# Performance work log

Hardware: AMD Instinct MI355X
Metric: run time of the kernel (lower is better)

## Reference

```python
import jax, jax.numpy as jnp
import numpy as np

T, B, E, H, V = 128, 64, 300, 2048, 50000


def setup_inputs() -> dict:
    key = jax.random.key(0)
    ks = jax.random.split(key, 7)
    tokens = jax.random.randint(ks[0], (T, B), 0, V, dtype=jnp.int32)
    lens = jax.random.randint(ks[1], (B,), 1, T + 1, dtype=jnp.int32)  # lens >= 1 (assert 0 not in lens)
    embed_table = jax.random.normal(ks[2], (V, E), dtype=jnp.float32) * 0.1
    W_ih = jax.random.normal(ks[3], (4 * H, E), dtype=jnp.float32) * 0.02
    W_hh = jax.random.normal(ks[4], (4 * H, H), dtype=jnp.float32) * 0.02
    b_ih = jax.random.normal(ks[5], (4 * H,), dtype=jnp.float32) * 0.02
    b_hh = jax.random.normal(ks[6], (4 * H,), dtype=jnp.float32) * 0.02
    return {"tokens": tokens, "lens": lens, "embed_table": embed_table,
            "W_ih": W_ih, "W_hh": W_hh, "b_ih": b_ih, "b_hh": b_hh}


def _lstm_scan(xs, W_ih, W_hh, bias, reverse):
    # xs: [T, B, E]; returns all hidden states [T, B, H] (in scan order) and final (h, c)
    hdim = W_hh.shape[1]
    bsz = xs.shape[1]
    h0 = jnp.zeros((bsz, hdim), xs.dtype)
    c0 = jnp.zeros((bsz, hdim), xs.dtype)

    def step(carry, x):
        h, c = carry
        gates = x @ W_ih.T + h @ W_hh.T + bias  # [B, 4H]
        i, f, g, o = jnp.split(gates, 4, axis=-1)  # PyTorch LSTMCell gate order: i, f, g, o
        i = jax.nn.sigmoid(i)
        f = jax.nn.sigmoid(f)
        g = jnp.tanh(g)
        o = jax.nn.sigmoid(o)
        c = f * c + i * g
        h = o * jnp.tanh(c)
        return (h, c), h

    (h_fin, c_fin), hs = jax.lax.scan(step, (h0, c0), xs, reverse=reverse)
    return hs, h_fin


def reference(tokens, lens, embed_table, W_ih, W_hh, b_ih, b_hh):
    # tokens: [T, B] int ids (time-major, matching input_[i] loop over dim 0)
    x = embed_table[tokens]  # [T, B, E]
    bias = b_ih + b_hh
    hs_fwd, _ = _lstm_scan(x, W_ih, W_hh, bias, reverse=False)   # [T, B, H]
    _, h_bwd = _lstm_scan(x, W_ih, W_hh, bias, reverse=True)     # [B, H], same shared cell
    bsz = tokens.shape[1]
    # forward hidden at the last valid timestep of each example (lens - 1)
    last_fwd = hs_fwd[lens - 1, jnp.arange(bsz)]  # [B, H]
    return jnp.concatenate([last_fwd, h_bwd], axis=1)  # [B, 2H]
```

## Files before the change

### kernel.cpp

```cpp
#include <hip/hip_runtime.h>
#include <math.h>

#define T_ 128
#define B_ 64
#define E_ 300
#define H_ 2048

#define K1   2368
#define XKS  10
#define NKS  74
#define APELEMS 19398656ull
#define BXELEMS 5242880ull
#define BHPING  524288ull

typedef __attribute__((ext_vector_type(8))) short short8;
typedef __attribute__((ext_vector_type(4))) float float4v;

__device__ __forceinline__ unsigned f2bf(float f) {
    unsigned u = __float_as_uint(f);
    return (u + 0x7FFFu + ((u >> 16) & 1u)) >> 16;
}
__device__ __forceinline__ float bf2f(unsigned b) { return __uint_as_float(b << 16); }

__device__ __forceinline__ void gl_lds16(const void* g, void* l) {
    __builtin_amdgcn_global_load_lds(
        (const __attribute__((address_space(1))) unsigned int*)g,
        (__attribute__((address_space(3))) unsigned int*)l, 16, 0, 0);
}

__device__ __forceinline__ float sigm(float x) { return 1.f / (1.f + expf(-x)); }


__global__ void init2(short* __restrict__ Bh, float* __restrict__ cb) {
    const int nB = 2 * (int)BHPING;
    const int nC = 2 * 2048 * 64;
    int stride = gridDim.x * blockDim.x;
    int i = blockIdx.x * blockDim.x + threadIdx.x;
    for (int idx = i; idx < nB; idx += stride) Bh[idx] = 0;
    for (int idx = i; idx < nC; idx += stride) cb[idx] = 0.f;
}

__global__ void pack_w(const float* __restrict__ Wih, const float* __restrict__ Whh,
                       short* __restrict__ Ahi, short* __restrict__ Alo) {
    long long idx = (long long)blockIdx.x * blockDim.x + threadIdx.x;
    if (idx >= (long long)APELEMS) return;
    int j  = (int)(idx & 7);
    int l  = (int)((idx >> 3) & 63);
    int mf = (int)((idx >> 9) & 7);
    int rest = (int)(idx >> 12);
    int ks = rest % 74;
    int rb = rest / 74;
    int row = rb * 128 + mf * 16 + (l & 15);
    int kr  = ks * 32 + (l >> 4) * 8 + j;
    float wv = 0.f;
    if (kr < 300)       wv = Wih[(size_t)row * 300 + kr];
    else if (kr >= 320) wv = Whh[(size_t)row * 2048 + (kr - 320)];
    unsigned hb = f2bf(wv);
    Ahi[idx] = (short)hb;
    Alo[idx] = (short)f2bf(wv - bf2f(hb));
}

__global__ void pack_x(const int* __restrict__ tokens, const float* __restrict__ embed,
                       short* __restrict__ Bx) {
    long long idx = (long long)blockIdx.x * blockDim.x + threadIdx.x;
    if (idx >= (long long)BXELEMS) return;
    int j   = (int)(idx & 7);
    int l   = (int)((idx >> 3) & 63);
    int nf4 = (int)((idx >> 9) & 3);
    int hl  = (int)((idx >> 11) & 1);
    int rest = (int)(idx >> 12);
    int ks = rest % 10;
    int tt = rest / 10;
    int b  = nf4 * 16 + (l & 15);
    int kr = ks * 32 + (l >> 4) * 8 + j;
    float v = 0.f;
    if (kr < 300) {
        int tok = tokens[tt * 64 + b];
        v = embed[(size_t)tok * 300 + kr];
    }
    unsigned hb = f2bf(v);
    Bx[idx] = hl ? (short)f2bf(v - bf2f(hb)) : (short)hb;
}

__global__ __launch_bounds__(256, 2) void gemm_step(
    const short* __restrict__ Ahi, const short* __restrict__ Alo,
    const short* __restrict__ Bx, const short* __restrict__ Bh,
    float* __restrict__ p, int t)
{
    __shared__ short lds[24576];
    const int bb = (int)blockIdx.x;
    const int mb = bb >> 2, s = bb & 3;
    const int rb = mb >> 1, half = mb & 1;
    const int tid = (int)threadIdx.x;
    const int w = tid >> 6, l = tid & 63;
    const int wm = w >> 1, wn = w & 1;
    const int ping = t & 1;
    const int ks0 = (s < 2) ? s * 19 : 38 + (s - 2) * 18;
    const int nks = (s < 2) ? 19 : 18;
    const short* AhiB = Ahi + (size_t)rb * 74 * 4096 + half * 2048;
    const short* AloB = Alo + (size_t)rb * 74 * 4096 + half * 2048;
    const short* BhP  = Bh + (size_t)ping * BHPING;

    float4v acc[2][4];
#pragma unroll
    for (int i = 0; i < 2; ++i)
#pragma unroll
        for (int n = 0; n < 4; ++n) acc[i][n] = (float4v){0.f, 0.f, 0.f, 0.f};

    auto stage = [&](int ks, int buf) {
        short* As = lds + buf * 12288;
        short* Al = As + 2048;
        short* Bs = As + 4096;
        gl_lds16(AhiB + (size_t)ks * 4096 + tid * 8, As + tid * 8);
        gl_lds16(AloB + (size_t)ks * 4096 + tid * 8, Al + tid * 8);
#pragma unroll
        for (int q = 0; q < 4; ++q) {
            const int dsel = q >> 1, hl = q & 1;
            const short* base;
            if (ks < XKS) {
                const int xt = dsel ? (127 - t) : t;
                base = Bx + (size_t)(((xt * 10 + ks) * 2 + hl) * 4) * 512;
            } else {
                base = BhP + (size_t)((ks - 10) * 16 + (dsel * 2 + hl) * 4) * 512;
            }
            gl_lds16(base + tid * 8, Bs + q * 2048 + tid * 8);
        }
    };

    stage(ks0, 0);
    for (int it = 0; it < nks; ++it) {
        asm volatile("s_waitcnt vmcnt(0)" ::: "memory");
        __builtin_amdgcn_s_barrier();
        __builtin_amdgcn_sched_barrier(0);

        short* As = lds + (it & 1) * 12288;
        short* Al = As + 2048;
        short* Bs = As + 4096;
        short8 ah[2], al[2], bf[8];
#pragma unroll
        for (int i = 0; i < 2; ++i) {
            ah[i] = *(const short8*)(As + ((wm * 2 + i) * 64 + l) * 8);
            al[i] = *(const short8*)(Al + ((wm * 2 + i) * 64 + l) * 8);
        }
#pragma unroll
        for (int j = 0; j < 8; ++j)
            bf[j] = *(const short8*)(Bs + ((wn * 8 + j) * 64 + l) * 8);

        stage(ks0 + it + 1, (it + 1) & 1);

        __builtin_amdgcn_s_setprio(1);
#pragma unroll
        for (int i = 0; i < 2; ++i)
#pragma unroll
            for (int h2 = 0; h2 < 2; ++h2)
#pragma unroll
                for (int n = 0; n < 4; ++n)
                    acc[i][n] = __builtin_amdgcn_mfma_f32_16x16x32_bf16(
                        ah[i], bf[h2 * 4 + n], acc[i][n], 0, 0, 0);
#pragma unroll
        for (int i = 0; i < 2; ++i)
#pragma unroll
            for (int n = 0; n < 4; ++n)
                acc[i][n] = __builtin_amdgcn_mfma_f32_16x16x32_bf16(
                    al[i], bf[n], acc[i][n], 0, 0, 0);
        __builtin_amdgcn_s_setprio(0);
    }
    asm volatile("s_waitcnt vmcnt(0)" ::: "memory");
    __builtin_amdgcn_s_barrier();
    __builtin_amdgcn_sched_barrier(0);

#pragma unroll
    for (int i = 0; i < 2; ++i)
#pragma unroll
        for (int n = 0; n < 4; ++n)
#pragma unroll
            for (int r = 0; r < 4; ++r) {
                int row = mb * 64 + wm * 32 + i * 16 + (l >> 4) * 4 + r;
                int col = wn * 64 + n * 16 + (l & 15);
                p[((size_t)s * 8192 + row) * 128 + col] = acc[i][n][r];
            }
}

__global__ __launch_bounds__(256) void update2(
    const float* __restrict__ p,
    const float* __restrict__ b_ih, const float* __restrict__ b_hh,
    const int* __restrict__ lens,
    float* __restrict__ cbuf,
    short* __restrict__ Bh,
    float* __restrict__ out, int t)
{
    int tid0 = blockIdx.x * 256 + threadIdx.x;
    for (int item = tid0; item < 262144; item += 65536) {
        int b = item & 63, k = (item >> 6) & 2047, dir = item >> 17;
        float g[4];
#pragma unroll
        for (int gg = 0; gg < 4; ++gg) {
            int row = gg * 2048 + k;
            float v = 0.f;
#pragma unroll
            for (int s = 0; s < 4; ++s) v += p[((size_t)s * 8192 + row) * 128 + dir * 64 + b];
            g[gg] = v + b_ih[row] + b_hh[row];
        }
        float iv = sigm(g[0]);
        float fv = sigm(g[1]);
        float gv = tanhf(g[2]);
        float ov = sigm(g[3]);
        size_t cidx = ((size_t)dir * 2048 + k) * 64 + b;
        float c = fv * cbuf[cidx] + iv * gv;
        cbuf[cidx] = c;
        float h = ov * tanhf(c);

        int kk = k & 31, ksh = k >> 5;
        int jj = kk & 7, ll = (kk >> 3) * 16 + (b & 15), sub = b >> 4;
        int pingW = (t + 1) & 1;
        size_t baseh = (size_t)pingW * BHPING + ((size_t)ksh * 16 + (dir * 2) * 4 + sub) * 512 + ll * 8 + jj;
        size_t basel = (size_t)pingW * BHPING + ((size_t)ksh * 16 + (dir * 2 + 1) * 4 + sub) * 512 + ll * 8 + jj;
        unsigned hb = f2bf(h);
        Bh[baseh] = (short)hb;
        Bh[basel] = (short)f2bf(h - bf2f(hb));

        if (dir == 0) { if (t == lens[b] - 1) out[(size_t)b * 4096 + k] = h; }
        else          { if (t == 127)         out[(size_t)b * 4096 + 2048 + k] = h; }
    }
}

__global__ void init_state(float* __restrict__ hbuf, float* __restrict__ cbuf) {
    int n_h = 2 * 2 * H_ * B_;
    int n_c = 2 * H_ * B_;
    int stride = gridDim.x * blockDim.x;
    int i = blockIdx.x * blockDim.x + threadIdx.x;
    for (int idx = i; idx < n_h; idx += stride) hbuf[idx] = 0.f;
    for (int idx = i; idx < n_c; idx += stride) cbuf[idx] = 0.f;
}

__global__ void gather_x(const int* __restrict__ tokens, const float* __restrict__ embed,
                         float* __restrict__ x_t) {
    int idx = blockIdx.x * blockDim.x + threadIdx.x;
    int total = T_ * E_ * B_;
    if (idx >= total) return;
    int b = idx % B_;
    int r = idx / B_;
    int e = r % E_;
    int t = r / E_;
    int tok = tokens[t * B_ + b];
    x_t[idx] = embed[tok * E_ + e];
}

__global__ __launch_bounds__(256) void lstm_step(
    const float* __restrict__ x_t, const float* __restrict__ W_ih,
    const float* __restrict__ W_hh, const float* __restrict__ b_ih,
    const float* __restrict__ b_hh, const int* __restrict__ lens,
    const float* __restrict__ h_in, float* __restrict__ h_out,
    float* __restrict__ cbuf, float* __restrict__ out, int t)
{
    const int dir = blockIdx.x >> 8;
    const int kblk = blockIdx.x & 255;
    const int bpair = threadIdx.x & 31;
    const int kloc = threadIdx.x >> 5;
    const int k = kblk * 8 + kloc;
    const int b0 = bpair * 2;
    const int xt = dir ? (T_ - 1 - t) : t;
    const float* xrow = x_t + (size_t)xt * E_ * B_;
    const float* hrow = h_in + (size_t)dir * H_ * B_;
    float a0x = 0.f, a0y = 0.f, a1x = 0.f, a1y = 0.f;
    float a2x = 0.f, a2y = 0.f, a3x = 0.f, a3y = 0.f;
    {
        const float* w0 = W_ih + (size_t)(0 * H_ + k) * E_;
        const float* w1 = W_ih + (size_t)(1 * H_ + k) * E_;
        const float* w2 = W_ih + (size_t)(2 * H_ + k) * E_;
        const float* w3 = W_ih + (size_t)(3 * H_ + k) * E_;
#pragma unroll 4
        for (int kk = 0; kk < E_; ++kk) {
            float2 xv = *(const float2*)(xrow + kk * B_ + b0);
            float c0 = w0[kk], c1 = w1[kk], c2 = w2[kk], c3 = w3[kk];
            a0x += xv.x * c0; a0y += xv.y * c0;
            a1x += xv.x * c1; a1y += xv.y * c1;
            a2x += xv.x * c2; a2y += xv.y * c2;
            a3x += xv.x * c3; a3y += xv.y * c3;
        }
    }
    {
        const float* w0 = W_hh + (size_t)(0 * H_ + k) * H_;
        const float* w1 = W_hh + (size_t)(1 * H_ + k) * H_;
        const float* w2 = W_hh + (size_t)(2 * H_ + k) * H_;
        const float* w3 = W_hh + (size_t)(3 * H_ + k) * H_;
#pragma unroll 4
        for (int kk = 0; kk < H_; ++kk) {
            float2 hv = *(const float2*)(hrow + kk * B_ + b0);
            float c0 = w0[kk], c1 = w1[kk], c2 = w2[kk], c3 = w3[kk];
            a0x += hv.x * c0; a0y += hv.y * c0;
            a1x += hv.x * c1; a1y += hv.y * c1;
            a2x += hv.x * c2; a2y += hv.y * c2;
            a3x += hv.x * c3; a3y += hv.y * c3;
        }
    }
    const int j0 = 0 * H_ + k, j1 = 1 * H_ + k, j2 = 2 * H_ + k, j3 = 3 * H_ + k;
    const float bi = b_ih[j0] + b_hh[j0];
    const float bf = b_ih[j1] + b_hh[j1];
    const float bg = b_ih[j2] + b_hh[j2];
    const float bo = b_ih[j3] + b_hh[j3];
    float* cdir = cbuf + (size_t)dir * H_ * B_;
    float* hdir = h_out + (size_t)dir * H_ * B_;
#pragma unroll
    for (int s = 0; s < 2; ++s) {
        const int b = b0 + s;
        const float ai = (s == 0) ? a0x : a0y;
        const float af = (s == 0) ? a1x : a1y;
        const float ag = (s == 0) ? a2x : a2y;
        const float ao = (s == 0) ? a3x : a3y;
        const float iv = sigm(ai + bi);
        const float fv = sigm(af + bf);
        const float gv = tanhf(ag + bg);
        const float ov = sigm(ao + bo);
        const int sidx = k * B_ + b;
        const float c_old = cdir[sidx];
        const float c_new = fv * c_old + iv * gv;
        cdir[sidx] = c_new;
        const float h_new = ov * tanhf(c_new);
        hdir[sidx] = h_new;
        if (dir == 0) {
            if (t == lens[b] - 1) out[(size_t)b * (2 * H_) + k] = h_new;
        } else {
            if (t == T_ - 1) out[(size_t)b * (2 * H_) + H_ + k] = h_new;
        }
    }
}

extern "C" void kernel_launch(void* const* d_in, const int* in_sizes, int n_in,
                              void* d_out, int out_size, void* d_ws, size_t ws_size,
                              hipStream_t stream) {
    const int*   tokens = (const int*)d_in[0];
    const int*   lens   = (const int*)d_in[1];
    const float* embed  = (const float*)d_in[2];
    const float* W_ih   = (const float*)d_in[3];
    const float* W_hh   = (const float*)d_in[4];
    const float* b_ih   = (const float*)d_in[5];
    const float* b_hh   = (const float*)d_in[6];
    float* out = (float*)d_out;

    short* Ahi = (short*)d_ws;
    short* Alo = Ahi + APELEMS;
    short* BxP = Alo + APELEMS;
    short* BhP = BxP + BXELEMS;
    float* cb2n = (float*)(BhP + 2 * BHPING);
    float* pP   = cb2n + 262144;
    const size_t req_new = (size_t)((char*)(pP + 4194304) - (char*)d_ws);

    float* ws   = (float*)d_ws;
    float* x_t  = ws;
    float* hbuf1 = x_t + (size_t)T_ * E_ * B_;
    float* cbuf1 = hbuf1 + (size_t)2 * 2 * H_ * B_;

    if (ws_size >= req_new) {
        init2<<<512, 256, 0, stream>>>(BhP, cb2n);
        pack_w<<<(int)((APELEMS + 255) / 256), 256, 0, stream>>>(W_ih, W_hh, Ahi, Alo);
        pack_x<<<(int)((BXELEMS + 255) / 256), 256, 0, stream>>>(tokens, embed, BxP);
        for (int t = 0; t < T_; ++t) {
            gemm_step<<<512, 256, 0, stream>>>(Ahi, Alo, BxP, BhP, pP, t);
            update2<<<256, 256, 0, stream>>>(pP, b_ih, b_hh, lens, cb2n, BhP, out, t);
        }
    } else {
        init_state<<<256, 256, 0, stream>>>(hbuf1, cbuf1);
        {
            int total = T_ * E_ * B_;
            gather_x<<<(total + 255) / 256, 256, 0, stream>>>(tokens, embed, x_t);
        }
        for (int t = 0; t < T_; ++t) {
            const float* h_in  = hbuf1 + (size_t)(t & 1) * 2 * H_ * B_;
            float*       h_out = hbuf1 + (size_t)((t + 1) & 1) * 2 * H_ * B_;
            lstm_step<<<512, 256, 0, stream>>>(x_t, W_ih, W_hh, b_ih, b_hh, lens,
                                               h_in, h_out, cbuf1, out, t);
        }
    }
}
```

Baseline: 3.395 ms.

## Compute the weight low-residual correction term with scaled FP8 MFMA

The bf16 low part of the weights (the residual after bf16 rounding) is now stored as scaled e4m3 FP8, and the Alo*Bhi correction product runs through fp8 MFMA into a separate accumulator that is rescaled and added at the end. Separate fp8 copies of the x and h high parts are produced by pack_x and update2 for this purpose. The aim is to halve the bytes loaded for the Alo operand and to use the faster fp8 MFMA, at the cost of extra fp8 conversion work in update2, more LDS, and lower precision in the correction term.

After: 3.537 ms. 4.2% more time.

```diff
diff --git a/kernel.cpp b/kernel.cpp
--- a/kernel.cpp
+++ b/kernel.cpp
@@ -11,7 +11,11 @@
 #define NKS  74
 #define APELEMS 19398656ull
 #define BXELEMS 5242880ull
+#define BXFBYTES 2621440ull
 #define BHPING  524288ull
+#define BHFPING 262144ull
+#define LOSCALE 16384.f
+#define LOINV   6.103515625e-05f
 
 typedef __attribute__((ext_vector_type(8))) short short8;
 typedef __attribute__((ext_vector_type(4))) float float4v;
@@ -21,6 +25,25 @@
     return (u + 0x7FFFu + ((u >> 16) & 1u)) >> 16;
 }
 __device__ __forceinline__ float bf2f(unsigned b) { return __uint_as_float(b << 16); }
+
+__device__ __forceinline__ unsigned char f2e4m3(float f) {
+    unsigned u = __float_as_uint(f);
+    unsigned s = (u >> 31) << 7;
+    u &= 0x7FFFFFFFu;
+    float a = __uint_as_float(u);
+    if (a >= 448.f) return (unsigned char)(s | 0x7E);
+    int e = (int)(u >> 23) - 127;
+    if (e < -6) {
+        int k = (int)(a * 512.f + 0.5f);
+        return (unsigned char)(s | (k <= 7 ? k : 8));
+    }
+    unsigned m = u & 0x7FFFFFu;
+    unsigned mr = m + 0x7FFFFu + ((m >> 20) & 1u);
+    if (mr >> 23) { mr = 0; e += 1; if (e > 8) return (unsigned char)(s | 0x7E); }
+    unsigned mm = (mr >> 20) & 7u;
+    if (e == 8 && mm == 7u) return (unsigned char)(s | 0x7E);
+    return (unsigned char)(s | ((unsigned)(e + 7) << 3) | mm);
+}
 
 __device__ __forceinline__ void gl_lds16(const void* g, void* l) {
     __builtin_amdgcn_global_load_lds(
@@ -31,17 +54,20 @@
 __device__ __forceinline__ float sigm(float x) { return 1.f / (1.f + expf(-x)); }
 
 
-__global__ void init2(short* __restrict__ Bh, float* __restrict__ cb) {
+__global__ void init2(short* __restrict__ Bh, unsigned char* __restrict__ BhF,
+                      float* __restrict__ cb) {
     const int nB = 2 * (int)BHPING;
+    const int nF = 2 * (int)BHFPING;
     const int nC = 2 * 2048 * 64;
     int stride = gridDim.x * blockDim.x;
     int i = blockIdx.x * blockDim.x + threadIdx.x;
     for (int idx = i; idx < nB; idx += stride) Bh[idx] = 0;
+    for (int idx = i; idx < nF; idx += stride) BhF[idx] = 0;
     for (int idx = i; idx < nC; idx += stride) cb[idx] = 0.f;
 }
 
 __global__ void pack_w(const float* __restrict__ Wih, const float* __restrict__ Whh,
-                       short* __restrict__ Ahi, short* __restrict__ Alo) {
+                       short* __restrict__ Ahi, unsigned char* __restrict__ AloF) {
     long long idx = (long long)blockIdx.x * blockDim.x + threadIdx.x;
     if (idx >= (long long)APELEMS) return;
     int j  = (int)(idx & 7);
@@ -57,11 +83,11 @@
     else if (kr >= 320) wv = Whh[(size_t)row * 2048 + (kr - 320)];
     unsigned hb = f2bf(wv);
     Ahi[idx] = (short)hb;
-    Alo[idx] = (short)f2bf(wv - bf2f(hb));
+    AloF[idx] = f2e4m3((wv - bf2f(hb)) * LOSCALE);
 }
 
 __global__ void pack_x(const int* __restrict__ tokens, const float* __restrict__ embed,
-                       short* __restrict__ Bx) {
+                       short* __restrict__ Bx, unsigned char* __restrict__ BxF) {
     long long idx = (long long)blockIdx.x * blockDim.x + threadIdx.x;
     if (idx >= (long long)BXELEMS) return;
     int j   = (int)(idx & 7);
@@ -79,15 +105,20 @@
         v = embed[(size_t)tok * 300 + kr];
     }
     unsigned hb = f2bf(v);
-    Bx[idx] = hl ? (short)f2bf(v - bf2f(hb)) : (short)hb;
+    if (hl) Bx[idx] = (short)f2bf(v - bf2f(hb));
+    else {
+        Bx[idx] = (short)hb;
+        BxF[(((size_t)(tt * 10 + ks) * 4 + nf4) * 64 + l) * 8 + j] = f2e4m3(bf2f(hb));
+    }
 }
 
 __global__ __launch_bounds__(256, 2) void gemm_step(
-    const short* __restrict__ Ahi, const short* __restrict__ Alo,
-    const short* __restrict__ Bx, const short* __restrict__ Bh,
+    const short* __restrict__ Ahi, const unsigned char* __restrict__ AloF,
+    const short* __restrict__ Bx, const unsigned char* __restrict__ BxF,
+    const short* __restrict__ Bh, const unsigned char* __restrict__ BhF,
     float* __restrict__ p, int t)
 {
-    __shared__ short lds[24576];
+    __shared__ short lds[26624];
     const int bb = (int)blockIdx.x;
     const int mb = bb >> 2, s = bb & 3;
     const int rb = mb >> 1, half = mb & 1;
@@ -98,21 +129,27 @@
     const int ks0 = (s < 2) ? s * 19 : 38 + (s - 2) * 18;
     const int nks = (s < 2) ? 19 : 18;
     const short* AhiB = Ahi + (size_t)rb * 74 * 4096 + half * 2048;
-    const short* AloB = Alo + (size_t)rb * 74 * 4096 + half * 2048;
+    const unsigned char* AloB = AloF + (size_t)rb * 74 * 4096 + half * 2048;
     const short* BhP  = Bh + (size_t)ping * BHPING;
-
-    float4v acc[2][4];
+    const unsigned char* BhFP = BhF + (size_t)ping * BHFPING;
+
+    float4v acc[2][4], acc8[2][4];
 #pragma unroll
     for (int i = 0; i < 2; ++i)
 #pragma unroll
-        for (int n = 0; n < 4; ++n) acc[i][n] = (float4v){0.f, 0.f, 0.f, 0.f};
+        for (int n = 0; n < 4; ++n) {
+            acc[i][n]  = (float4v){0.f, 0.f, 0.f, 0.f};
+            acc8[i][n] = (float4v){0.f, 0.f, 0.f, 0.f};
+        }
 
     auto stage = [&](int ks, int buf) {
-        short* As = lds + buf * 12288;
-        short* Al = As + 2048;
-        short* Bs = As + 4096;
+        short* As = lds + buf * 13312;
+        char*  Al8 = (char*)(As + 2048);
+        short* Bs = As + 3072;
+        char*  Bl8 = (char*)(As + 11264);
         gl_lds16(AhiB + (size_t)ks * 4096 + tid * 8, As + tid * 8);
-        gl_lds16(AloB + (size_t)ks * 4096 + tid * 8, Al + tid * 8);
+        if (tid < 128)
+            gl_lds16(AloB + (size_t)ks * 4096 + tid * 16, Al8 + tid * 16);
 #pragma unroll
         for (int q = 0; q < 4; ++q) {
             const int dsel = q >> 1, hl = q & 1;
@@ -125,6 +162,15 @@
             }
             gl_lds16(base + tid * 8, Bs + q * 2048 + tid * 8);
         }
+        const unsigned char* srcl;
+        if (ks < XKS) {
+            const int dsel = tid >> 7;
+            const int xt = dsel ? (127 - t) : t;
+            srcl = BxF + (size_t)((xt * 10 + ks) * 4) * 512 + (tid & 127) * 16;
+        } else {
+            srcl = BhFP + (size_t)((ks - 10) * 8) * 512 + tid * 16;
+        }
+        gl_lds16(srcl, Bl8 + tid * 16);
     };
 
     stage(ks0, 0);
@@ -133,18 +179,23 @@
         __builtin_amdgcn_s_barrier();
         __builtin_amdgcn_sched_barrier(0);
 
-        short* As = lds + (it & 1) * 12288;
-        short* Al = As + 2048;
-        short* Bs = As + 4096;
-        short8 ah[2], al[2], bf[8];
+        short* As = lds + (it & 1) * 13312;
+        char*  Al8 = (char*)(As + 2048);
+        short* Bs = As + 3072;
+        char*  Bl8 = (char*)(As + 11264);
+        short8 ah[2], bf[8];
+        long   al8[2], bl8[4];
 #pragma unroll
         for (int i = 0; i < 2; ++i) {
-            ah[i] = *(const short8*)(As + ((wm * 2 + i) * 64 + l) * 8);
-            al[i] = *(const short8*)(Al + ((wm * 2 + i) * 64 + l) * 8);
+            ah[i]  = *(const short8*)(As + ((wm * 2 + i) * 64 + l) * 8);
+            al8[i] = *(const long*)(Al8 + ((wm * 2 + i) * 64 + l) * 8);
         }
 #pragma unroll
         for (int j = 0; j < 8; ++j)
             bf[j] = *(const short8*)(Bs + ((wn * 8 + j) * 64 + l) * 8);
+#pragma unroll
+        for (int n = 0; n < 4; ++n)
+            bl8[n] = *(const long*)(Bl8 + ((wn * 4 + n) * 64 + l) * 8);
 
         stage(ks0 + it + 1, (it + 1) & 1);
 
@@ -161,8 +212,8 @@
         for (int i = 0; i < 2; ++i)
 #pragma unroll
             for (int n = 0; n < 4; ++n)
-                acc[i][n] = __builtin_amdgcn_mfma_f32_16x16x32_bf16(
-                    al[i], bf[n], acc[i][n], 0, 0, 0);
+                acc8[i][n] = __builtin_amdgcn_mfma_f32_16x16x32_fp8_fp8(
+                    al8[i], bl8[n], acc8[i][n], 0, 0, 0);
         __builtin_amdgcn_s_setprio(0);
     }
     asm volatile("s_waitcnt vmcnt(0)" ::: "memory");
@@ -177,7 +228,8 @@
             for (int r = 0; r < 4; ++r) {
                 int row = mb * 64 + wm * 32 + i * 16 + (l >> 4) * 4 + r;
                 int col = wn * 64 + n * 16 + (l & 15);
-                p[((size_t)s * 8192 + row) * 128 + col] = acc[i][n][r];
+                p[((size_t)s * 8192 + row) * 128 + col] =
+                    acc[i][n][r] + acc8[i][n][r] * LOINV;
             }
 }
 
@@ -186,7 +238,7 @@
     const float* __restrict__ b_ih, const float* __restrict__ b_hh,
     const int* __restrict__ lens,
     float* __restrict__ cbuf,
-    short* __restrict__ Bh,
+    short* __restrict__ Bh, unsigned char* __restrict__ BhF,
     float* __restrict__ out, int t)
 {
     int tid0 = blockIdx.x * 256 + threadIdx.x;
@@ -218,6 +270,8 @@
         unsigned hb = f2bf(h);
         Bh[baseh] = (short)hb;
         Bh[basel] = (short)f2bf(h - bf2f(hb));
+        BhF[(size_t)pingW * BHFPING + ((size_t)ksh * 8 + dir * 4 + sub) * 512 + ll * 8 + jj]
+            = f2e4m3(bf2f(hb));
 
         if (dir == 0) { if (t == lens[b] - 1) out[(size_t)b * 4096 + k] = h; }
         else          { if (t == 127)         out[(size_t)b * 4096 + 2048 + k] = h; }
@@ -339,10 +393,12 @@
     float* out = (float*)d_out;
 
     short* Ahi = (short*)d_ws;
-    short* Alo = Ahi + APELEMS;
-    short* BxP = Alo + APELEMS;
-    short* BhP = BxP + BXELEMS;
-    float* cb2n = (float*)(BhP + 2 * BHPING);
+    unsigned char* AloF = (unsigned char*)(Ahi + APELEMS);
+    short* BxP = (short*)(AloF + APELEMS);
+    unsigned char* BxF = (unsigned char*)(BxP + BXELEMS);
+    short* BhP = (short*)(BxF + BXFBYTES);
+    unsigned char* BhF = (unsigned char*)(BhP + 2 * BHPING);
+    float* cb2n = (float*)(BhF + 2 * BHFPING);
     float* pP   = cb2n + 262144;
     const size_t req_new = (size_t)((char*)(pP + 4194304) - (char*)d_ws);
 
@@ -352,12 +408,12 @@
     float* cbuf1 = hbuf1 + (size_t)2 * 2 * H_ * B_;
 
     if (ws_size >= req_new) {
-        init2<<<512, 256, 0, stream>>>(BhP, cb2n);
-        pack_w<<<(int)((APELEMS + 255) / 256), 256, 0, stream>>>(W_ih, W_hh, Ahi, Alo);
-        pack_x<<<(int)((BXELEMS + 255) / 256), 256, 0, stream>>>(tokens, embed, BxP);
+        init2<<<512, 256, 0, stream>>>(BhP, BhF, cb2n);
+        pack_w<<<(int)((APELEMS + 255) / 256), 256, 0, stream>>>(W_ih, W_hh, Ahi, AloF);
+        pack_x<<<(int)((BXELEMS + 255) / 256), 256, 0, stream>>>(tokens, embed, BxP, BxF);
         for (int t = 0; t < T_; ++t) {
-            gemm_step<<<512, 256, 0, stream>>>(Ahi, Alo, BxP, BhP, pP, t);
-            update2<<<256, 256, 0, stream>>>(pP, b_ih, b_hh, lens, cb2n, BhP, out, t);
+            gemm_step<<<512, 256, 0, stream>>>(Ahi, AloF, BxP, BxF, BhP, BhF, pP, t);
+            update2<<<256, 256, 0, stream>>>(pP, b_ih, b_hh, lens, cb2n, BhP, BhF, out, t);
         }
     } else {
         init_state<<<256, 256, 0, stream>>>(hbuf1, cbuf1);
```
